# Performance work log

Measured on AMD Instinct MI355X. Metric: run time of the kernel, lower is better.

Reference implementation:

```python
import jax, jax.numpy as jnp
import numpy as np

R, N1, N2, D = 4, 4096, 4096, 8


def setup_inputs() -> dict:
    key = jax.random.key(0)
    k1, k2, k3 = jax.random.split(key, 3)
    x1 = jax.random.normal(k1, (R, N1, D), dtype=jnp.float32)
    x2 = jax.random.normal(k2, (R, N2, D), dtype=jnp.float32)
    # learned parameters (init: ones), matching nn.Parameter(torch.ones(...))
    lengthscales = jnp.ones((D, 1), dtype=jnp.float32)
    output_scale = jnp.ones((1,), dtype=jnp.float32)
    return {"x1": x1, "x2": x2, "lengthscales": lengthscales, "output_scale": output_scale}


def reference(x1, x2, lengthscales, output_scale):
    # RBF.K: output_scale^2 * exp(-0.5 * sum_d ((x1 - x2) / lengthscales)^2)
    # Computed via the Gram identity ||a-b||^2 = ||a||^2 + ||b||^2 - 2 a.b
    inv_ls = 1.0 / lengthscales.reshape(-1)          # [D]
    a = x1 * inv_ls                                  # [R, N1, D]
    b = x2 * inv_ls                                  # [R, N2, D]
    aa = jnp.sum(a * a, axis=-1)                     # [R, N1]
    bb = jnp.sum(b * b, axis=-1)                     # [R, N2]
    ab = jnp.einsum('rnd,rmd->rnm', a, b)            # [R, N1, N2]
    sqdist = jnp.maximum(aa[:, :, None] + bb[:, None, :] - 2.0 * ab, 0.0)
    return (output_scale[0] ** 2) * jnp.exp(-0.5 * sqdist)
```

## Files before the change

### kernel.cpp

```cpp
#include <hip/hip_runtime.h>


constexpr int D  = 8;
constexpr int BI = 64;
constexpr int BJ = 64;

__global__ __launch_bounds__(256, 4) void rbf_kernel(
    const float* __restrict__ x1, const float* __restrict__ x2,
    const float* __restrict__ ls, const float* __restrict__ osc,
    float* __restrict__ out, int N1, int N2)
{
    __shared__ float sa[BI][D];
    __shared__ float sb[D][BJ];

    const int r   = blockIdx.z;
    const int i0  = blockIdx.y * BI;
    const int j0  = blockIdx.x * BJ;
    const int tid = threadIdx.x;

    const int t  = tid & 127;
    const int pt = t >> 1;
    const int hf = t & 1;

    float4 lsv = *reinterpret_cast<const float4*>(ls + hf * 4);
    float4 inv;
    inv.x = 1.0f / lsv.x; inv.y = 1.0f / lsv.y;
    inv.z = 1.0f / lsv.z; inv.w = 1.0f / lsv.w;

    if (tid < 128) {
        const float* src = x1 + ((size_t)r * N1 + (i0 + pt)) * D + hf * 4;
        float4 v = *reinterpret_cast<const float4*>(src);
        v.x *= inv.x; v.y *= inv.y; v.z *= inv.z; v.w *= inv.w;
        *reinterpret_cast<float4*>(&sa[pt][hf * 4]) = v;
    } else {
        const float* src = x2 + ((size_t)r * N2 + (j0 + pt)) * D + hf * 4;
        float4 v = *reinterpret_cast<const float4*>(src);
        v.x *= inv.x; v.y *= inv.y; v.z *= inv.z; v.w *= inv.w;
        sb[hf * 4 + 0][pt] = v.x;
        sb[hf * 4 + 1][pt] = v.y;
        sb[hf * 4 + 2][pt] = v.z;
        sb[hf * 4 + 3][pt] = v.w;
    }
    const float os2 = osc[0] * osc[0];
    __syncthreads();

    const int tx = tid & 15;
    const int ty = tid >> 4;

    float4 b[D];
#pragma unroll
    for (int d = 0; d < D; ++d)
        b[d] = *reinterpret_cast<const float4*>(&sb[d][tx * 4]);

    float a[4][D];
#pragma unroll
    for (int ii = 0; ii < 4; ++ii) {
#pragma unroll
        for (int h = 0; h < 2; ++h) {
            float4 v = *reinterpret_cast<const float4*>(&sa[ty * 4 + ii][h * 4]);
            a[ii][h * 4 + 0] = v.x; a[ii][h * 4 + 1] = v.y;
            a[ii][h * 4 + 2] = v.z; a[ii][h * 4 + 3] = v.w;
        }
    }

#pragma unroll
    for (int ii = 0; ii < 4; ++ii) {
        float s0 = 0.f, s1 = 0.f, s2 = 0.f, s3 = 0.f;
#pragma unroll
        for (int d = 0; d < D; ++d) {
            const float  av = a[ii][d];
            const float4 bv = b[d];
            const float d0 = av - bv.x, d1 = av - bv.y;
            const float d2 = av - bv.z, d3 = av - bv.w;
            s0 = fmaf(d0, d0, s0); s1 = fmaf(d1, d1, s1);
            s2 = fmaf(d2, d2, s2); s3 = fmaf(d3, d3, s3);
        }
        float4 o;
        o.x = os2 * __expf(-0.5f * s0);
        o.y = os2 * __expf(-0.5f * s1);
        o.z = os2 * __expf(-0.5f * s2);
        o.w = os2 * __expf(-0.5f * s3);
        const int i = i0 + ty * 4 + ii;
        *reinterpret_cast<float4*>(out + ((size_t)r * N1 + i) * N2 + j0 + tx * 4) = o;
    }
}

extern "C" void kernel_launch(void* const* d_in, const int* in_sizes, int n_in,
                              void* d_out, int out_size, void* d_ws, size_t ws_size,
                              hipStream_t stream) {
    (void)in_sizes; (void)n_in; (void)d_ws; (void)ws_size; (void)out_size;
    const float* x1  = (const float*)d_in[0];
    const float* x2  = (const float*)d_in[1];
    const float* ls  = (const float*)d_in[2];
    const float* osc = (const float*)d_in[3];
    float* out = (float*)d_out;

    const int R = 4, N1 = 4096, N2 = 4096;
    dim3 grid(N2 / BJ, N1 / BI, R);
    rbf_kernel<<<grid, dim3(256), 0, stream>>>(x1, x2, ls, osc, out, N1, N2);
}
```

Baseline: 55.05 us.

## Use Gram identity with precomputed norms, exp2 builtin, and 16x256 tiles

Replaces the per-element difference-square loop with a dot product plus precomputed squared norms folded into a single FMA feeding a native exp2. It also reshapes the tile to 16 rows by 256 columns so each wavefront writes a full contiguous 1 KB row segment, and raises the occupancy hint. The goal is fewer ALU ops per output and wider coalesced stores in this store-bound kernel. It drops the max(.,0) clamp, so rounding can push the exponent slightly positive, and loading each x2 tile in more, smaller blocks raises redundant input traffic.

```diff
diff --git a/kernel.cpp b/kernel.cpp
--- a/kernel.cpp
+++ b/kernel.cpp
@@ -2,86 +2,104 @@
 
 
 constexpr int D  = 8;
-constexpr int BI = 64;
-constexpr int BJ = 64;
+constexpr int BI = 16;
+constexpr int BJ = 256;
 
-__global__ __launch_bounds__(256, 4) void rbf_kernel(
+#if __has_builtin(__builtin_amdgcn_exp2f)
+#define FAST_EXP2(x) __builtin_amdgcn_exp2f(x)
+#else
+#define FAST_EXP2(x) __expf((x) * 0.69314718f)
+#endif
+
+__global__ __launch_bounds__(256, 6) void rbf_kernel(
     const float* __restrict__ x1, const float* __restrict__ x2,
     const float* __restrict__ ls, const float* __restrict__ osc,
     float* __restrict__ out, int N1, int N2)
 {
+    __shared__ float sb[D][BJ];
+    __shared__ float sbb[BJ];
     __shared__ float sa[BI][D];
-    __shared__ float sb[D][BJ];
+    __shared__ float sasq[BI];
 
     const int r   = blockIdx.z;
     const int i0  = blockIdx.y * BI;
     const int j0  = blockIdx.x * BJ;
     const int tid = threadIdx.x;
 
-    const int t  = tid & 127;
-    const int pt = t >> 1;
-    const int hf = t & 1;
+    float4 l0 = *reinterpret_cast<const float4*>(ls);
+    float4 l1 = *reinterpret_cast<const float4*>(ls + 4);
+    float4 inv0, inv1;
+    inv0.x = 1.0f / l0.x; inv0.y = 1.0f / l0.y; inv0.z = 1.0f / l0.z; inv0.w = 1.0f / l0.w;
+    inv1.x = 1.0f / l1.x; inv1.y = 1.0f / l1.y; inv1.z = 1.0f / l1.z; inv1.w = 1.0f / l1.w;
 
-    float4 lsv = *reinterpret_cast<const float4*>(ls + hf * 4);
-    float4 inv;
-    inv.x = 1.0f / lsv.x; inv.y = 1.0f / lsv.y;
-    inv.z = 1.0f / lsv.z; inv.w = 1.0f / lsv.w;
-
-    if (tid < 128) {
-        const float* src = x1 + ((size_t)r * N1 + (i0 + pt)) * D + hf * 4;
-        float4 v = *reinterpret_cast<const float4*>(src);
-        v.x *= inv.x; v.y *= inv.y; v.z *= inv.z; v.w *= inv.w;
-        *reinterpret_cast<float4*>(&sa[pt][hf * 4]) = v;
-    } else {
-        const float* src = x2 + ((size_t)r * N2 + (j0 + pt)) * D + hf * 4;
-        float4 v = *reinterpret_cast<const float4*>(src);
-        v.x *= inv.x; v.y *= inv.y; v.z *= inv.z; v.w *= inv.w;
-        sb[hf * 4 + 0][pt] = v.x;
-        sb[hf * 4 + 1][pt] = v.y;
-        sb[hf * 4 + 2][pt] = v.z;
-        sb[hf * 4 + 3][pt] = v.w;
+    {
+        const float* src = x2 + ((size_t)r * N2 + j0 + tid) * D;
+        float4 v0 = *reinterpret_cast<const float4*>(src);
+        float4 v1 = *reinterpret_cast<const float4*>(src + 4);
+        v0.x *= inv0.x; v0.y *= inv0.y; v0.z *= inv0.z; v0.w *= inv0.w;
+        v1.x *= inv1.x; v1.y *= inv1.y; v1.z *= inv1.z; v1.w *= inv1.w;
+        sb[0][tid] = v0.x; sb[1][tid] = v0.y; sb[2][tid] = v0.z; sb[3][tid] = v0.w;
+        sb[4][tid] = v1.x; sb[5][tid] = v1.y; sb[6][tid] = v1.z; sb[7][tid] = v1.w;
+        sbb[tid] = v0.x*v0.x + v0.y*v0.y + v0.z*v0.z + v0.w*v0.w
+                 + v1.x*v1.x + v1.y*v1.y + v1.z*v1.z + v1.w*v1.w;
+    }
+    if (tid < BI) {
+        const float* src = x1 + ((size_t)r * N1 + i0 + tid) * D;
+        float4 v0 = *reinterpret_cast<const float4*>(src);
+        float4 v1 = *reinterpret_cast<const float4*>(src + 4);
+        v0.x *= inv0.x; v0.y *= inv0.y; v0.z *= inv0.z; v0.w *= inv0.w;
+        v1.x *= inv1.x; v1.y *= inv1.y; v1.z *= inv1.z; v1.w *= inv1.w;
+        *reinterpret_cast<float4*>(&sa[tid][0]) = v0;
+        *reinterpret_cast<float4*>(&sa[tid][4]) = v1;
+        sasq[tid] = v0.x*v0.x + v0.y*v0.y + v0.z*v0.z + v0.w*v0.w
+                  + v1.x*v1.x + v1.y*v1.y + v1.z*v1.z + v1.w*v1.w;
     }
     const float os2 = osc[0] * osc[0];
     __syncthreads();
 
-    const int tx = tid & 15;
-    const int ty = tid >> 4;
+    const int lane = tid & 63;
+    const int wv   = tid >> 6;
 
-    float4 b[D];
+    float4 bd[D];
 #pragma unroll
     for (int d = 0; d < D; ++d)
-        b[d] = *reinterpret_cast<const float4*>(&sb[d][tx * 4]);
+        bd[d] = *reinterpret_cast<const float4*>(&sb[d][lane * 4]);
+    const float4 bb4 = *reinterpret_cast<const float4*>(&sbb[lane * 4]);
 
-    float a[4][D];
-#pragma unroll
-    for (int ii = 0; ii < 4; ++ii) {
-#pragma unroll
-        for (int h = 0; h < 2; ++h) {
-            float4 v = *reinterpret_cast<const float4*>(&sa[ty * 4 + ii][h * 4]);
-            a[ii][h * 4 + 0] = v.x; a[ii][h * 4 + 1] = v.y;
-            a[ii][h * 4 + 2] = v.z; a[ii][h * 4 + 3] = v.w;
-        }
-    }
+    constexpr float L2E  = 1.44269504f;
+    constexpr float NH2E = -0.72134752f;
+
+    float* obase = out + ((size_t)r * N1 + i0) * (size_t)N2 + j0 + lane * 4;
 
 #pragma unroll
     for (int ii = 0; ii < 4; ++ii) {
-        float s0 = 0.f, s1 = 0.f, s2 = 0.f, s3 = 0.f;
+        const int row = wv * 4 + ii;
+        const float4 a0  = *reinterpret_cast<const float4*>(&sa[row][0]);
+        const float4 a1  = *reinterpret_cast<const float4*>(&sa[row][4]);
+        const float  asq = sasq[row];
+
+        float4 ch;
+        ch.x = (asq + bb4.x) * NH2E;
+        ch.y = (asq + bb4.y) * NH2E;
+        ch.z = (asq + bb4.z) * NH2E;
+        ch.w = (asq + bb4.w) * NH2E;
+
+        float d0 = 0.f, d1 = 0.f, d2 = 0.f, d3 = 0.f;
+        const float a[D] = {a0.x, a0.y, a0.z, a0.w, a1.x, a1.y, a1.z, a1.w};
 #pragma unroll
         for (int d = 0; d < D; ++d) {
-            const float  av = a[ii][d];
-            const float4 bv = b[d];
-            const float d0 = av - bv.x, d1 = av - bv.y;
-            const float d2 = av - bv.z, d3 = av - bv.w;
-            s0 = fmaf(d0, d0, s0); s1 = fmaf(d1, d1, s1);
-            s2 = fmaf(d2, d2, s2); s3 = fmaf(d3, d3, s3);
+            const float av = a[d];
+            d0 = fmaf(av, bd[d].x, d0);
+            d1 = fmaf(av, bd[d].y, d1);
+            d2 = fmaf(av, bd[d].z, d2);
+            d3 = fmaf(av, bd[d].w, d3);
         }
         float4 o;
-        o.x = os2 * __expf(-0.5f * s0);
-        o.y = os2 * __expf(-0.5f * s1);
-        o.z = os2 * __expf(-0.5f * s2);
-        o.w = os2 * __expf(-0.5f * s3);
-        const int i = i0 + ty * 4 + ii;
-        *reinterpret_cast<float4*>(out + ((size_t)r * N1 + i) * N2 + j0 + tx * 4) = o;
+        o.x = os2 * FAST_EXP2(fmaf(d0, L2E, ch.x));
+        o.y = os2 * FAST_EXP2(fmaf(d1, L2E, ch.y));
+        o.z = os2 * FAST_EXP2(fmaf(d2, L2E, ch.z));
+        o.w = os2 * FAST_EXP2(fmaf(d3, L2E, ch.w));
+        *reinterpret_cast<float4*>(obase + (size_t)row * N2) = o;
     }
 }
 
```

Result: faster. 51.04 us (-7.3%).
